# Kernel tuning notes

Measured on AMD Instinct MI355X. Metric: run time of the kernel, lower is better.

The kernel has to match this reference:

```python
import jax, jax.numpy as jnp
import numpy as np

B, T, D_MODEL, N_HEADS, N_KV = 2, 2048, 1024, 16, 4
HEAD = D_MODEL // N_HEADS  # 64
NEG_INF = -1e9


def sine_table(features, length):
    # standard RoPE frequency table: theta_i = 10000^(2i/d)
    fraction = jnp.arange(0, features, 2, dtype=jnp.float32) / features
    timescale = 10000.0 ** fraction  # (features/2,)
    sinusoid = jnp.arange(length, dtype=jnp.float32)[:, None] / timescale[None, :]
    sinusoid = jnp.concatenate([sinusoid, sinusoid], axis=-1)  # (L, features)
    return jnp.sin(sinusoid), jnp.cos(sinusoid)


def rotate_half(x):
    x1, x2 = jnp.split(x, 2, axis=-1)
    return jnp.concatenate([-x2, x1], axis=-1)


def apply_rope(x, sin, cos):
    # x: (B, H, T, D); sin/cos: (L, D)
    t = x.shape[-2]
    return x * cos[:t][None, None] + rotate_half(x) * sin[:t][None, None]


def setup_inputs() -> dict:
    key = jax.random.key(0)
    k1, k2, k3, k4 = jax.random.split(key, 4)
    return {
        'q': jax.random.normal(k1, (B, T, D_MODEL), dtype=jnp.float32),
        'k': jax.random.normal(k2, (B, T, N_KV * HEAD), dtype=jnp.float32),
        'v': jax.random.normal(k3, (B, T, N_KV * HEAD), dtype=jnp.float32),
        'w_out': jax.random.normal(k4, (D_MODEL, D_MODEL), dtype=jnp.float32) * 0.02,
    }


def reference(q, k, v, w_out):
    Bq, Tq, C = q.shape
    head = C // N_HEADS
    # split heads: q -> (B, n_heads, T, head); k/v -> (B, n_kv, T, head)
    qh = q.reshape(Bq, Tq, N_HEADS, head).transpose(0, 2, 1, 3)
    kh = k.reshape(Bq, Tq, N_KV, head).transpose(0, 2, 1, 3)
    vh = v.reshape(Bq, Tq, N_KV, head).transpose(0, 2, 1, 3)
    # inline RoPE on q and k
    sin, cos = sine_table(head, Tq)
    qh = apply_rope(qh, sin, cos)
    kh = apply_rope(kh, sin, cos)
    # GQA repeat of kv heads to match q heads
    rep = N_HEADS // N_KV
    kh = jnp.repeat(kh, rep, axis=1)
    vh = jnp.repeat(vh, rep, axis=1)
    # manual scaled-dot-product attention with causal masking (full T^2 logits)
    logits = jnp.einsum('bhqd,bhkd->bhqk', qh, kh) / jnp.sqrt(jnp.float32(head))
    causal = jnp.tril(jnp.ones((Tq, Tq), dtype=jnp.float32))
    logits = jnp.where(causal == 0, NEG_INF, logits)
    attn = jax.nn.softmax(logits, axis=-1)
    out = jnp.einsum('bhqk,bhkd->bhqd', attn, vh)
    out = out.transpose(0, 2, 1, 3).reshape(Bq, Tq, C)
    return out @ w_out
```

## Files before the change

kernel.cpp:

```cpp
#include <hip/hip_runtime.h>
#include <math.h>

#define T_SEQ 2048
#define NH    16
#define NKV   4

typedef __attribute__((ext_vector_type(8)))  _Float16 f16x8;
typedef __attribute__((ext_vector_type(4)))  _Float16 f16x4;
typedef __attribute__((ext_vector_type(2)))  __fp16   fp16x2b;
typedef __attribute__((ext_vector_type(4)))  float    f32x4;

#if __has_builtin(__builtin_amdgcn_exp2f)
#define EXP2F(x) __builtin_amdgcn_exp2f(x)
#else
#define EXP2F(x) exp2f(x)
#endif

#define QSCALE 0.18033688011112042f

#define LDS_BARRIER()                                        \
    do {                                                     \
        __builtin_amdgcn_sched_barrier(0);                   \
        asm volatile("s_waitcnt lgkmcnt(0)" ::: "memory");   \
        __builtin_amdgcn_s_barrier();                        \
        __builtin_amdgcn_sched_barrier(0);                   \
    } while (0)

__global__ __launch_bounds__(256) void prep_kernel(const float* __restrict__ k,
                                                   const float* __restrict__ v,
                                                   const float* __restrict__ w,
                                                   float2* __restrict__ tb,
                                                   _Float16* __restrict__ Kr,
                                                   _Float16* __restrict__ Vt,
                                                   _Float16* __restrict__ Wt)
{
    __shared__ _Float16 L[64 * 72];
    const int bx = blockIdx.x;
    if (bx < 256) {
        int idx = bx * 256 + threadIdx.x;
        int i = idx & 31, t = idx >> 5;
        float inv = __expf((float)i * (-9.210340371976184f / 32.0f));
        float ang = (float)t * inv;
        tb[idx] = make_float2(cosf(ang), sinf(ang));
    } else if (bx < 512) {
        int idx = (bx - 256) * 256 + threadIdx.x;
        int i   = idx & 31;
        int t   = idx >> 5;
        float inv = __expf((float)i * (-9.210340371976184f / 32.0f));
        float ang = (float)t * inv;
        float sn = sinf(ang), cs = cosf(ang);
        #pragma unroll
        for (int bk = 0; bk < 8; ++bk) {
            const float* src = k + ((size_t)(bk >> 2) * T_SEQ + t) * 256 + (bk & 3) * 64 + i;
            float x1 = src[0], x2 = src[32];
            _Float16* dst = Kr + ((size_t)bk * T_SEQ + t) * 64 + i;
            dst[0]  = (_Float16)(x1 * cs - x2 * sn);
            dst[32] = (_Float16)(x2 * cs + x1 * sn);
        }
    } else if (bx < 768) {
        const int id = bx - 512;
        const int t0 = (id & 31) * 64, bk = id >> 5;
        const int b = bk >> 2, kh = bk & 3;
        const int rr = threadIdx.x >> 2, pp = threadIdx.x & 3;
        const float* src = v + ((size_t)(b * T_SEQ + t0 + rr)) * 256 + kh * 64 + pp * 16;
        f32x4 s0 = *(const f32x4*)(src), s1 = *(const f32x4*)(src + 4);
        f32x4 s2 = *(const f32x4*)(src + 8), s3 = *(const f32x4*)(src + 12);
        _Float16* lp = &L[rr * 72 + pp * 16];
        #pragma unroll
        for (int j = 0; j < 4; ++j) { lp[j] = (_Float16)s0[j]; lp[4+j] = (_Float16)s1[j];
                                      lp[8+j] = (_Float16)s2[j]; lp[12+j] = (_Float16)s3[j]; }
        __syncthreads();
        f16x8 w0, w1;
        #pragma unroll
        for (int j = 0; j < 8; ++j) w0[j] = L[(pp * 16 + j) * 72 + rr];
        #pragma unroll
        for (int j = 0; j < 8; ++j) w1[j] = L[(pp * 16 + 8 + j) * 72 + rr];
        _Float16* dst = Vt + ((size_t)bk * 64 + rr) * T_SEQ + t0 + pp * 16;
        *(f16x8*)dst = w0; *(f16x8*)(dst + 8) = w1;
    } else {
        const int id = bx - 768;
        const int k0 = (id & 15) * 64, n0 = (id >> 4) * 64;
        const int rr = threadIdx.x >> 2, pp = threadIdx.x & 3;
        const float* src = w + (size_t)(k0 + rr) * 1024 + n0 + pp * 16;
        f32x4 s0 = *(const f32x4*)(src), s1 = *(const f32x4*)(src + 4);
        f32x4 s2 = *(const f32x4*)(src + 8), s3 = *(const f32x4*)(src + 12);
        _Float16* lp = &L[rr * 72 + pp * 16];
        #pragma unroll
        for (int j = 0; j < 4; ++j) { lp[j] = (_Float16)s0[j]; lp[4+j] = (_Float16)s1[j];
                                      lp[8+j] = (_Float16)s2[j]; lp[12+j] = (_Float16)s3[j]; }
        __syncthreads();
        f16x8 w0, w1;
        #pragma unroll
        for (int j = 0; j < 8; ++j) w0[j] = L[(pp * 16 + j) * 72 + rr];
        #pragma unroll
        for (int j = 0; j < 8; ++j) w1[j] = L[(pp * 16 + 8 + j) * 72 + rr];
        _Float16* dst = Wt + (size_t)(n0 + rr) * 1024 + k0 + pp * 16;
        *(f16x8*)dst = w0; *(f16x8*)(dst + 8) = w1;
    }
}


__global__ __launch_bounds__(256) void attn_kernel(const float* __restrict__ q,
                                                   const float2* __restrict__ tb,
                                                   const _Float16* __restrict__ Kr,
                                                   const _Float16* __restrict__ Vt,
                                                   _Float16* __restrict__ AO)
{
    __shared__ _Float16 smem[32768];

    const int wid  = threadIdx.x >> 6;
    const int lane = threadIdx.x & 63;
    const int bh = blockIdx.x & 31;
    const int pp = blockIdx.x >> 5;
    const int p  = (pp < 8) ? pp : (23 - pp);
    const int qb0 = p, qb1 = 31 - p;
    const int b = bh >> 4, h = bh & 15;
    const int kh = h >> 2;
    const int bkh = b * NKV + kh;
    const int g = lane >> 4, r = lane & 15;
    const int NT = qb1 + 1;
    const int npair = NT >> 1;

    const int srow   = wid * 16 + (lane >> 3);
    const int schunk = lane & 7;
    const _Float16* kgbase = Kr + (size_t)bkh * T_SEQ * 64;
    const _Float16* vgbase = Vt + (size_t)bkh * 64 * T_SEQ;
    const int kd0 = srow * 64 + ((schunk ^ (srow & 7)) * 8);
    const int kd1 = kd0 + 8 * 64;

    f16x8 sKa0, sKa1, sVa0, sVa1, sKb0, sKb1, sVb0, sVb1;
    {
        const _Float16* kg = kgbase + (size_t)srow * 64 + schunk * 8;
        sKa0 = *(const f16x8*)(kg);
        sKa1 = *(const f16x8*)(kg + 8 * 64);
        sKb0 = *(const f16x8*)(kg + 4096);
        sKb1 = *(const f16x8*)(kg + 4096 + 8 * 64);
        const _Float16* vg = vgbase + (size_t)srow * T_SEQ + schunk * 8;
        sVa0 = *(const f16x8*)(vg);
        sVa1 = *(const f16x8*)(vg + 8 * T_SEQ);
        sVb0 = *(const f16x8*)(vg + 64);
        sVb1 = *(const f16x8*)(vg + 8 * T_SEQ + 64);
    }

    f16x8 qa[2][2];
    #pragma unroll
    for (int tl = 0; tl < 2; ++tl) {
        const int t = (tl ? qb1 : qb0) * 64 + wid * 16 + r;
        const float* qs = q + ((size_t)b * T_SEQ + t) * 1024 + h * 64 + 8 * g;
        const float2* tp = tb + t * 32 + 8 * g;
        #pragma unroll
        for (int j = 0; j < 8; ++j) {
            float x0 = qs[j], x1 = qs[32 + j];
            float2 cs = tp[j];
            qa[tl][0][j] = (_Float16)((x0 * cs.x - x1 * cs.y) * QSCALE);
            qa[tl][1][j] = (_Float16)((x1 * cs.x + x0 * cs.y) * QSCALE);
        }
    }

    {
        _Float16* kw = smem;
        _Float16* vw = smem + 8192;
        *(f16x8*)(&kw[kd0]) = sKa0;        *(f16x8*)(&kw[kd1]) = sKa1;
        *(f16x8*)(&kw[4096 + kd0]) = sKb0; *(f16x8*)(&kw[4096 + kd1]) = sKb1;
        *(f16x8*)(&vw[kd0]) = sVa0;        *(f16x8*)(&vw[kd1]) = sVa1;
        *(f16x8*)(&vw[4096 + kd0]) = sVb0; *(f16x8*)(&vw[4096 + kd1]) = sVb1;
        const _Float16* kg = kgbase + (size_t)(128 + srow) * 64 + schunk * 8;
        sKa0 = *(const f16x8*)(kg);
        sKa1 = *(const f16x8*)(kg + 8 * 64);
        sKb0 = *(const f16x8*)(kg + 4096);
        sKb1 = *(const f16x8*)(kg + 4096 + 8 * 64);
        const _Float16* vg = vgbase + (size_t)srow * T_SEQ + 128 + schunk * 8;
        sVa0 = *(const f16x8*)(vg);
        sVa1 = *(const f16x8*)(vg + 8 * T_SEQ);
        sVb0 = *(const f16x8*)(vg + 64);
        sVb1 = *(const f16x8*)(vg + 8 * T_SEQ + 64);
    }
    LDS_BARRIER();

    f32x4 o[2][4];
    f32x4 o4[2];
    #pragma unroll
    for (int tl = 0; tl < 2; ++tl) {
        #pragma unroll
        for (int db = 0; db < 4; ++db) o[tl][db] = (f32x4){0.f,0.f,0.f,0.f};
        o4[tl] = (f32x4){0.f,0.f,0.f,0.f};
    }
    const f16x4 onesf = {(_Float16)1.f, (_Float16)1.f, (_Float16)1.f, (_Float16)1.f};

    auto tile_body = [&](int kvb, const _Float16* ks, const _Float16* vs) {
        const bool act0 = (kvb <= qb0);
        f32x4 stt[2][4];
        __builtin_amdgcn_s_setprio(1);
        #pragma unroll
        for (int kt = 0; kt < 4; ++kt) {
            f16x8 ka0 = *(const f16x8*)(ks + (kt*16 + r) * 64 + ((g       ^ (r & 7)) * 8));
            f16x8 ka1 = *(const f16x8*)(ks + (kt*16 + r) * 64 + (((4 + g) ^ (r & 7)) * 8));
            f32x4 s1 = {0.f,0.f,0.f,0.f};
            s1 = __builtin_amdgcn_mfma_f32_16x16x32_f16(ka0, qa[1][0], s1, 0, 0, 0);
            s1 = __builtin_amdgcn_mfma_f32_16x16x32_f16(ka1, qa[1][1], s1, 0, 0, 0);
            stt[1][kt] = s1;
            if (act0) {
                f32x4 s0 = {0.f,0.f,0.f,0.f};
                s0 = __builtin_amdgcn_mfma_f32_16x16x32_f16(ka0, qa[0][0], s0, 0, 0, 0);
                s0 = __builtin_amdgcn_mfma_f32_16x16x32_f16(ka1, qa[0][1], s0, 0, 0, 0);
                stt[0][kt] = s0;
            }
        }
        __builtin_amdgcn_s_setprio(0);

        if (kvb == qb0) {
            #pragma unroll
            for (int kt = 0; kt < 4; ++kt)
                #pragma unroll
                for (int j = 0; j < 4; ++j)
                    if (kt*16 + 4*g + j > wid*16 + r) stt[0][kt][j] = -1e9f;
        }
        if (kvb == qb1) {
            #pragma unroll
            for (int kt = 0; kt < 4; ++kt)
                #pragma unroll
                for (int j = 0; j < 4; ++j)
                    if (kt*16 + 4*g + j > wid*16 + r) stt[1][kt][j] = -1e9f;
        }

        f16x4 pf[2][4];
        #pragma unroll
        for (int tl = 0; tl < 2; ++tl) {
            if (tl == 0 && !act0) continue;
            #pragma unroll
            for (int kt = 0; kt < 4; ++kt) {
                float p0 = EXP2F(stt[tl][kt][0]);
                float p1 = EXP2F(stt[tl][kt][1]);
                float p2 = EXP2F(stt[tl][kt][2]);
                float p3 = EXP2F(stt[tl][kt][3]);
                union { unsigned u[2]; f16x4 v; } pk;
                union { fp16x2b hh; unsigned u; } c0, c1;
                c0.hh = __builtin_amdgcn_cvt_pkrtz(p0, p1);
                c1.hh = __builtin_amdgcn_cvt_pkrtz(p2, p3);
                pk.u[0] = c0.u; pk.u[1] = c1.u;
                pf[tl][kt] = pk.v;
            }
        }

        __builtin_amdgcn_s_setprio(1);
        #pragma unroll
        for (int kt = 0; kt < 4; ++kt) {
            const int vc = ((2*kt + (g >> 1)) ^ (r & 7)) * 8 + (g & 1) * 4;
            f16x4 v0 = *(const f16x4*)(vs + (0*16 + r) * 64 + vc);
            f16x4 v1 = *(const f16x4*)(vs + (1*16 + r) * 64 + vc);
            f16x4 v2 = *(const f16x4*)(vs + (2*16 + r) * 64 + vc);
            f16x4 v3 = *(const f16x4*)(vs + (3*16 + r) * 64 + vc);
            o[1][0] = __builtin_amdgcn_mfma_f32_16x16x16f16(pf[1][kt], v0, o[1][0], 0, 0, 0);
            o[1][1] = __builtin_amdgcn_mfma_f32_16x16x16f16(pf[1][kt], v1, o[1][1], 0, 0, 0);
            o[1][2] = __builtin_amdgcn_mfma_f32_16x16x16f16(pf[1][kt], v2, o[1][2], 0, 0, 0);
            o[1][3] = __builtin_amdgcn_mfma_f32_16x16x16f16(pf[1][kt], v3, o[1][3], 0, 0, 0);
            o4[1]   = __builtin_amdgcn_mfma_f32_16x16x16f16(pf[1][kt], onesf, o4[1], 0, 0, 0);
            if (act0) {
                o[0][0] = __builtin_amdgcn_mfma_f32_16x16x16f16(pf[0][kt], v0, o[0][0], 0, 0, 0);
                o[0][1] = __builtin_amdgcn_mfma_f32_16x16x16f16(pf[0][kt], v1, o[0][1], 0, 0, 0);
                o[0][2] = __builtin_amdgcn_mfma_f32_16x16x16f16(pf[0][kt], v2, o[0][2], 0, 0, 0);
                o[0][3] = __builtin_amdgcn_mfma_f32_16x16x16f16(pf[0][kt], v3, o[0][3], 0, 0, 0);
                o4[0]   = __builtin_amdgcn_mfma_f32_16x16x16f16(pf[0][kt], onesf, o4[0], 0, 0, 0);
            }
        }
        __builtin_amdgcn_s_setprio(0);
    };

    for (int j = 0; j < npair; ++j) {
        const _Float16* kbuf = smem + (j & 1) * 16384;
        const _Float16* vbuf = kbuf + 8192;
        tile_body(2*j,     kbuf,        vbuf);
        tile_body(2*j + 1, kbuf + 4096, vbuf + 4096);

        const int t2 = 2*j + 2, t3 = 2*j + 3;
        _Float16* kw = smem + ((j + 1) & 1) * 16384;
        _Float16* vw = kw + 8192;
        if (t2 < NT) {
            *(f16x8*)(&kw[kd0]) = sKa0; *(f16x8*)(&kw[kd1]) = sKa1;
            *(f16x8*)(&vw[kd0]) = sVa0; *(f16x8*)(&vw[kd1]) = sVa1;
        }
        if (t3 < NT) {
            *(f16x8*)(&kw[4096 + kd0]) = sKb0; *(f16x8*)(&kw[4096 + kd1]) = sKb1;
            *(f16x8*)(&vw[4096 + kd0]) = sVb0; *(f16x8*)(&vw[4096 + kd1]) = sVb1;
        }
        const int t4 = 2*j + 4, t5 = 2*j + 5;
        if (t4 < NT) {
            const _Float16* kg = kgbase + (size_t)(t4 * 64 + srow) * 64 + schunk * 8;
            sKa0 = *(const f16x8*)(kg);
            sKa1 = *(const f16x8*)(kg + 8 * 64);
            const _Float16* vg = vgbase + (size_t)srow * T_SEQ + t4 * 64 + schunk * 8;
            sVa0 = *(const f16x8*)(vg);
            sVa1 = *(const f16x8*)(vg + 8 * T_SEQ);
        }
        if (t5 < NT) {
            const _Float16* kg = kgbase + (size_t)(t5 * 64 + srow) * 64 + schunk * 8;
            sKb0 = *(const f16x8*)(kg);
            sKb1 = *(const f16x8*)(kg + 8 * 64);
            const _Float16* vg = vgbase + (size_t)srow * T_SEQ + t5 * 64 + schunk * 8;
            sVb0 = *(const f16x8*)(vg);
            sVb1 = *(const f16x8*)(vg + 8 * T_SEQ);
        }
        LDS_BARRIER();
    }
    if (NT & 1) {
        const _Float16* kbuf = smem + (npair & 1) * 16384;
        tile_body(NT - 1, kbuf, kbuf + 8192);
    }

    __syncthreads();
    #pragma unroll
    for (int tl = 0; tl < 2; ++tl) {
        f32x4 li;
        #pragma unroll
        for (int j = 0; j < 4; ++j) li[j] = 1.0f / o4[tl][j];
        _Float16* Os = smem + tl * 4608;
        #pragma unroll
        for (int db = 0; db < 4; ++db) {
            f32x4 ov = o[tl][db] * li;
            #pragma unroll
            for (int j = 0; j < 4; ++j)
                Os[(wid*16 + 4*g + j) * 72 + db*16 + r] = (_Float16)ov[j];
        }
    }
    __syncthreads();
    {
        const int row = threadIdx.x >> 2, part = threadIdx.x & 3;
        #pragma unroll
        for (int tl = 0; tl < 2; ++tl) {
            const int qb = tl ? qb1 : qb0;
            const _Float16* src = smem + tl * 4608 + row * 72 + part * 16;
            _Float16* dst = AO + ((size_t)b * T_SEQ + qb * 64 + row) * 1024 + h * 64 + part * 16;
            *(f16x8*)dst       = *(const f16x8*)src;
            *(f16x8*)(dst + 8) = *(const f16x8*)(src + 8);
        }
    }
}


#define GST 72
__global__ __launch_bounds__(256) void gemm_kernel(const _Float16* __restrict__ A,
                                                   const _Float16* __restrict__ Bt,
                                                   float* __restrict__ C)
{
    __shared__ _Float16 As[2][128 * GST];
    __shared__ _Float16 Bs[2][64 * GST];
    const int tid  = threadIdx.x;
    const int by   = blockIdx.x & 31;
    const int bx   = blockIdx.x >> 5;
    const int lane = tid & 63;
    const int wid  = tid >> 6;
    const int g = lane >> 4, r = lane & 15;
    const int wm = wid >> 1, wn = wid & 1;

    f32x4 acc[4][2];
    #pragma unroll
    for (int i = 0; i < 4; ++i)
        #pragma unroll
        for (int j = 0; j < 2; ++j) acc[i][j] = (f32x4){0.f,0.f,0.f,0.f};

    size_t aoff[4], boff[2];
    int    ad[4], bd[2];
    #pragma unroll
    for (int i = 0; i < 4; ++i) {
        const int c = tid + 256 * i;
        aoff[i] = (size_t)(by*128 + (c >> 3)) * 1024 + (c & 7) * 8;
        ad[i]   = (c >> 3) * GST + (c & 7) * 8;
    }
    #pragma unroll
    for (int i = 0; i < 2; ++i) {
        const int c = tid + 256 * i;
        boff[i] = (size_t)(bx*64 + (c >> 3)) * 1024 + (c & 7) * 8;
        bd[i]   = (c >> 3) * GST + (c & 7) * 8;
    }

    {
        #pragma unroll
        for (int i = 0; i < 4; ++i)
            *(f16x8*)(&As[0][ad[i]]) = *(const f16x8*)(A + aoff[i]);
        #pragma unroll
        for (int i = 0; i < 2; ++i)
            *(f16x8*)(&Bs[0][bd[i]]) = *(const f16x8*)(Bt + boff[i]);
    }
    f16x8 sAB0, sAB1, sAB2, sAB3, sBB0, sBB1;
    f16x8 sAA0, sAA1, sAA2, sAA3, sBA0, sBA1;
    sAB0 = *(const f16x8*)(A  + aoff[0] + 64);
    sAB1 = *(const f16x8*)(A  + aoff[1] + 64);
    sAB2 = *(const f16x8*)(A  + aoff[2] + 64);
    sAB3 = *(const f16x8*)(A  + aoff[3] + 64);
    sBB0 = *(const f16x8*)(Bt + boff[0] + 64);
    sBB1 = *(const f16x8*)(Bt + boff[1] + 64);
    __syncthreads();

    auto iter_body = [&](int it,
                         f16x8& iA0, f16x8& iA1, f16x8& iA2, f16x8& iA3,
                         f16x8& iB0, f16x8& iB1,
                         f16x8& oA0, f16x8& oA1, f16x8& oA2, f16x8& oA3,
                         f16x8& oB0, f16x8& oB1) {
        if (it + 2 < 16) {
            const size_t ko = (size_t)(it + 2) * 64;
            iA0 = *(const f16x8*)(A  + aoff[0] + ko);
            iA1 = *(const f16x8*)(A  + aoff[1] + ko);
            iA2 = *(const f16x8*)(A  + aoff[2] + ko);
            iA3 = *(const f16x8*)(A  + aoff[3] + ko);
            iB0 = *(const f16x8*)(Bt + boff[0] + ko);
            iB1 = *(const f16x8*)(Bt + boff[1] + ko);
        }
        const int cur = it & 1;
        #pragma unroll
        for (int sub = 0; sub < 2; ++sub) {
            f16x8 af[4], bfv[2];
            #pragma unroll
            for (int mi = 0; mi < 4; ++mi)
                af[mi] = *(const f16x8*)(&As[cur][(wm*64 + mi*16 + r) * GST + sub*32 + 8*g]);
            #pragma unroll
            for (int ni = 0; ni < 2; ++ni)
                bfv[ni] = *(const f16x8*)(&Bs[cur][(wn*32 + ni*16 + r) * GST + sub*32 + 8*g]);
            __builtin_amdgcn_s_setprio(1);
            #pragma unroll
            for (int mi = 0; mi < 4; ++mi)
                #pragma unroll
                for (int ni = 0; ni < 2; ++ni)
                    acc[mi][ni] = __builtin_amdgcn_mfma_f32_16x16x32_f16(
                                      af[mi], bfv[ni], acc[mi][ni], 0, 0, 0);
            __builtin_amdgcn_s_setprio(0);
        }
        if (it + 1 < 16) {
            *(f16x8*)(&As[cur ^ 1][ad[0]]) = oA0;
            *(f16x8*)(&As[cur ^ 1][ad[1]]) = oA1;
            *(f16x8*)(&As[cur ^ 1][ad[2]]) = oA2;
            *(f16x8*)(&As[cur ^ 1][ad[3]]) = oA3;
            *(f16x8*)(&Bs[cur ^ 1][bd[0]]) = oB0;
            *(f16x8*)(&Bs[cur ^ 1][bd[1]]) = oB1;
        }
        LDS_BARRIER();
    };

    #pragma unroll 2
    for (int it = 0; it < 16; it += 2) {
        iter_body(it,     sAA0, sAA1, sAA2, sAA3, sBA0, sBA1,
                          sAB0, sAB1, sAB2, sAB3, sBB0, sBB1);
        iter_body(it + 1, sAB0, sAB1, sAB2, sAB3, sBB0, sBB1,
                          sAA0, sAA1, sAA2, sAA3, sBA0, sBA1);
    }

    #pragma unroll
    for (int mi = 0; mi < 4; ++mi)
        #pragma unroll
        for (int ni = 0; ni < 2; ++ni)
            #pragma unroll
            for (int j = 0; j < 4; ++j)
                C[(size_t)(by*128 + wm*64 + mi*16 + 4*g + j) * 1024
                  + bx*64 + wn*32 + ni*16 + r] = acc[mi][ni][j];
}


extern "C" void kernel_launch(void* const* d_in, const int* in_sizes, int n_in,
                              void* d_out, int out_size, void* d_ws, size_t ws_size,
                              hipStream_t stream) {
    const float* q = (const float*)d_in[0];
    const float* k = (const float*)d_in[1];
    const float* v = (const float*)d_in[2];
    const float* w = (const float*)d_in[3];
    float* out = (float*)d_out;

    char* ws = (char*)d_ws;
    float2*   tb = (float2*)(ws);
    _Float16* Kr = (_Float16*)(ws + ((size_t)1 << 20));
    _Float16* Vt = (_Float16*)(ws + ((size_t)3 << 20));
    _Float16* Wt = (_Float16*)(ws + ((size_t)5 << 20));
    _Float16* AO = (_Float16*)(ws + ((size_t)7 << 20));

    hipLaunchKernelGGL(prep_kernel,  dim3(1024), dim3(256), 0, stream, k, v, w, tb, Kr, Vt, Wt);
    hipLaunchKernelGGL(attn_kernel,  dim3(512),  dim3(256), 0, stream, q, tb, Kr, Vt, AO);
    hipLaunchKernelGGL(gemm_kernel,  dim3(512),  dim3(256), 0, stream, AO, Wt, out);
}
```

Before: 65.62 us.

## Read K and V directly from global memory instead of staging through LDS

Removes the double-buffered LDS staging of K/V tiles, the register prefetch pipeline and the per-pair barriers. Each wave now loads its K and V MFMA fragments straight from global memory and relies on the caches, since the four waves and the four query heads sharing a KV head reuse the same data. LDS shrinks to just the output staging buffer, which may raise occupancy. The cost is that each wave issues its own global loads with no prefetch overlap, and the V fragment loads are strided by the sequence length.

```diff
diff --git a/kernel.cpp b/kernel.cpp
--- a/kernel.cpp
+++ b/kernel.cpp
@@ -106,7 +106,7 @@
                                                    const _Float16* __restrict__ Vt,
                                                    _Float16* __restrict__ AO)
 {
-    __shared__ _Float16 smem[32768];
+    __shared__ _Float16 smem[9216];
 
     const int wid  = threadIdx.x >> 6;
     const int lane = threadIdx.x & 63;
@@ -118,29 +118,9 @@
     const int kh = h >> 2;
     const int bkh = b * NKV + kh;
     const int g = lane >> 4, r = lane & 15;
-    const int NT = qb1 + 1;
-    const int npair = NT >> 1;
-
-    const int srow   = wid * 16 + (lane >> 3);
-    const int schunk = lane & 7;
+
     const _Float16* kgbase = Kr + (size_t)bkh * T_SEQ * 64;
     const _Float16* vgbase = Vt + (size_t)bkh * 64 * T_SEQ;
-    const int kd0 = srow * 64 + ((schunk ^ (srow & 7)) * 8);
-    const int kd1 = kd0 + 8 * 64;
-
-    f16x8 sKa0, sKa1, sVa0, sVa1, sKb0, sKb1, sVb0, sVb1;
-    {
-        const _Float16* kg = kgbase + (size_t)srow * 64 + schunk * 8;
-        sKa0 = *(const f16x8*)(kg);
-        sKa1 = *(const f16x8*)(kg + 8 * 64);
-        sKb0 = *(const f16x8*)(kg + 4096);
-        sKb1 = *(const f16x8*)(kg + 4096 + 8 * 64);
-        const _Float16* vg = vgbase + (size_t)srow * T_SEQ + schunk * 8;
-        sVa0 = *(const f16x8*)(vg);
-        sVa1 = *(const f16x8*)(vg + 8 * T_SEQ);
-        sVb0 = *(const f16x8*)(vg + 64);
-        sVb1 = *(const f16x8*)(vg + 8 * T_SEQ + 64);
-    }
 
     f16x8 qa[2][2];
     #pragma unroll
@@ -157,26 +137,6 @@
         }
     }
 
-    {
-        _Float16* kw = smem;
-        _Float16* vw = smem + 8192;
-        *(f16x8*)(&kw[kd0]) = sKa0;        *(f16x8*)(&kw[kd1]) = sKa1;
-        *(f16x8*)(&kw[4096 + kd0]) = sKb0; *(f16x8*)(&kw[4096 + kd1]) = sKb1;
-        *(f16x8*)(&vw[kd0]) = sVa0;        *(f16x8*)(&vw[kd1]) = sVa1;
-        *(f16x8*)(&vw[4096 + kd0]) = sVb0; *(f16x8*)(&vw[4096 + kd1]) = sVb1;
-        const _Float16* kg = kgbase + (size_t)(128 + srow) * 64 + schunk * 8;
-        sKa0 = *(const f16x8*)(kg);
-        sKa1 = *(const f16x8*)(kg + 8 * 64);
-        sKb0 = *(const f16x8*)(kg + 4096);
-        sKb1 = *(const f16x8*)(kg + 4096 + 8 * 64);
-        const _Float16* vg = vgbase + (size_t)srow * T_SEQ + 128 + schunk * 8;
-        sVa0 = *(const f16x8*)(vg);
-        sVa1 = *(const f16x8*)(vg + 8 * T_SEQ);
-        sVb0 = *(const f16x8*)(vg + 64);
-        sVb1 = *(const f16x8*)(vg + 8 * T_SEQ + 64);
-    }
-    LDS_BARRIER();
-
     f32x4 o[2][4];
     f32x4 o4[2];
     #pragma unroll
@@ -187,14 +147,18 @@
     }
     const f16x4 onesf = {(_Float16)1.f, (_Float16)1.f, (_Float16)1.f, (_Float16)1.f};
 
-    auto tile_body = [&](int kvb, const _Float16* ks, const _Float16* vs) {
+    for (int kvb = 0; kvb <= qb1; ++kvb) {
         const bool act0 = (kvb <= qb0);
+        const _Float16* kb = kgbase + (size_t)(kvb * 64) * 64;
+        const _Float16* vb = vgbase + kvb * 64;
+
         f32x4 stt[2][4];
         __builtin_amdgcn_s_setprio(1);
         #pragma unroll
         for (int kt = 0; kt < 4; ++kt) {
-            f16x8 ka0 = *(const f16x8*)(ks + (kt*16 + r) * 64 + ((g       ^ (r & 7)) * 8));
-            f16x8 ka1 = *(const f16x8*)(ks + (kt*16 + r) * 64 + (((4 + g) ^ (r & 7)) * 8));
+            const _Float16* krow = kb + (kt * 16 + r) * 64 + 8 * g;
+            f16x8 ka0 = *(const f16x8*)(krow);
+            f16x8 ka1 = *(const f16x8*)(krow + 32);
             f32x4 s1 = {0.f,0.f,0.f,0.f};
             s1 = __builtin_amdgcn_mfma_f32_16x16x32_f16(ka0, qa[1][0], s1, 0, 0, 0);
             s1 = __builtin_amdgcn_mfma_f32_16x16x32_f16(ka1, qa[1][1], s1, 0, 0, 0);
@@ -245,11 +209,11 @@
         __builtin_amdgcn_s_setprio(1);
         #pragma unroll
         for (int kt = 0; kt < 4; ++kt) {
-            const int vc = ((2*kt + (g >> 1)) ^ (r & 7)) * 8 + (g & 1) * 4;
-            f16x4 v0 = *(const f16x4*)(vs + (0*16 + r) * 64 + vc);
-            f16x4 v1 = *(const f16x4*)(vs + (1*16 + r) * 64 + vc);
-            f16x4 v2 = *(const f16x4*)(vs + (2*16 + r) * 64 + vc);
-            f16x4 v3 = *(const f16x4*)(vs + (3*16 + r) * 64 + vc);
+            const _Float16* vc = vb + kt * 16 + 4 * g;
+            f16x4 v0 = *(const f16x4*)(vc + (size_t)(0*16 + r) * T_SEQ);
+            f16x4 v1 = *(const f16x4*)(vc + (size_t)(1*16 + r) * T_SEQ);
+            f16x4 v2 = *(const f16x4*)(vc + (size_t)(2*16 + r) * T_SEQ);
+            f16x4 v3 = *(const f16x4*)(vc + (size_t)(3*16 + r) * T_SEQ);
             o[1][0] = __builtin_amdgcn_mfma_f32_16x16x16f16(pf[1][kt], v0, o[1][0], 0, 0, 0);
             o[1][1] = __builtin_amdgcn_mfma_f32_16x16x16f16(pf[1][kt], v1, o[1][1], 0, 0, 0);
             o[1][2] = __builtin_amdgcn_mfma_f32_16x16x16f16(pf[1][kt], v2, o[1][2], 0, 0, 0);
@@ -264,50 +228,8 @@
             }
         }
         __builtin_amdgcn_s_setprio(0);
-    };
-
-    for (int j = 0; j < npair; ++j) {
-        const _Float16* kbuf = smem + (j & 1) * 16384;
-        const _Float16* vbuf = kbuf + 8192;
-        tile_body(2*j,     kbuf,        vbuf);
-        tile_body(2*j + 1, kbuf + 4096, vbuf + 4096);
-
-        const int t2 = 2*j + 2, t3 = 2*j + 3;
-        _Float16* kw = smem + ((j + 1) & 1) * 16384;
-        _Float16* vw = kw + 8192;
-        if (t2 < NT) {
-            *(f16x8*)(&kw[kd0]) = sKa0; *(f16x8*)(&kw[kd1]) = sKa1;
-            *(f16x8*)(&vw[kd0]) = sVa0; *(f16x8*)(&vw[kd1]) = sVa1;
-        }
-        if (t3 < NT) {
-            *(f16x8*)(&kw[4096 + kd0]) = sKb0; *(f16x8*)(&kw[4096 + kd1]) = sKb1;
-            *(f16x8*)(&vw[4096 + kd0]) = sVb0; *(f16x8*)(&vw[4096 + kd1]) = sVb1;
-        }
-        const int t4 = 2*j + 4, t5 = 2*j + 5;
-        if (t4 < NT) {
-            const _Float16* kg = kgbase + (size_t)(t4 * 64 + srow) * 64 + schunk * 8;
-            sKa0 = *(const f16x8*)(kg);
-            sKa1 = *(const f16x8*)(kg + 8 * 64);
-            const _Float16* vg = vgbase + (size_t)srow * T_SEQ + t4 * 64 + schunk * 8;
-            sVa0 = *(const f16x8*)(vg);
-            sVa1 = *(const f16x8*)(vg + 8 * T_SEQ);
-        }
-        if (t5 < NT) {
-            const _Float16* kg = kgbase + (size_t)(t5 * 64 + srow) * 64 + schunk * 8;
-            sKb0 = *(const f16x8*)(kg);
-            sKb1 = *(const f16x8*)(kg + 8 * 64);
-            const _Float16* vg = vgbase + (size_t)srow * T_SEQ + t5 * 64 + schunk * 8;
-            sVb0 = *(const f16x8*)(vg);
-            sVb1 = *(const f16x8*)(vg + 8 * T_SEQ);
-        }
-        LDS_BARRIER();
-    }
-    if (NT & 1) {
-        const _Float16* kbuf = smem + (npair & 1) * 16384;
-        tile_body(NT - 1, kbuf, kbuf + 8192);
-    }
-
-    __syncthreads();
+    }
+
     #pragma unroll
     for (int tl = 0; tl < 2; ++tl) {
         f32x4 li;
@@ -335,7 +257,6 @@
         }
     }
 }
-
 
 #define GST 72
 __global__ __launch_bounds__(256) void gemm_kernel(const _Float16* __restrict__ A,
```

Result: slower. 166.1 us (+153.1%).
